# Optimization experiments

Measured on AMD Instinct MI355X. Metric: run time of the kernel, lower is better.

Reference implementation:

```python
import jax, jax.numpy as jnp
import numpy as np

T = 2048       # tokens (flattened, single causal sequence)
HID = 2048     # hidden_size
H = 16         # num_heads
DN = 128       # qk_nope_head_dim
DR = 64        # qk_rope_head_dim
DV = 128       # v_head_dim
DQK = DN + DR  # 192
QLR = 1536     # q_lora_rank
KVLR = 512     # kv_lora_rank
THETA = 10000.0
EPS = 1e-6
SCALE = DQK ** -0.5


def rmsnorm(x, w):
    return x * jax.lax.rsqrt(jnp.mean(x * x, axis=-1, keepdims=True) + EPS) * w


def rope_interleaved(x, cos, sin):
    # is_neox_style=False: rotate interleaved even/odd pairs
    x1 = x[..., 0::2]
    x2 = x[..., 1::2]
    out = jnp.stack([x1 * cos - x2 * sin, x2 * cos + x1 * sin], axis=-1)
    return out.reshape(x.shape)


def setup_inputs() -> dict:
    key = jax.random.key(0)
    ks = jax.random.split(key, 8)
    s = 0.02
    return {
        "positions": jnp.arange(T, dtype=jnp.int32),
        "hidden_states": jax.random.normal(ks[0], (T, HID), jnp.float32),
        "w_q_a": jax.random.normal(ks[1], (HID, QLR), jnp.float32) * s,
        "q_a_ln_w": jnp.ones((QLR,), jnp.float32),
        "w_q_b": jax.random.normal(ks[2], (QLR, H * DQK), jnp.float32) * s,
        "w_kv_a": jax.random.normal(ks[3], (HID, KVLR + DR), jnp.float32) * s,
        "kv_a_ln_w": jnp.ones((KVLR,), jnp.float32),
        "w_kv_b": jax.random.normal(ks[4], (KVLR, H * (DN + DV)), jnp.float32) * s,
        "w_o": jax.random.normal(ks[5], (H * DV, HID), jnp.float32) * s,
    }


def reference(positions, hidden_states, w_q_a, q_a_ln_w, w_q_b, w_kv_a,
              kv_a_ln_w, w_kv_b, w_o):
    t = hidden_states.shape[0]
    # --- Q low-rank path ---
    q = rmsnorm(hidden_states @ w_q_a, q_a_ln_w) @ w_q_b          # [T, H*DQK]
    q = q.reshape(t, H, DQK)
    q_nope, q_pe = q[..., :DN], q[..., DN:]
    # --- KV latent path ---
    latent = hidden_states @ w_kv_a                                # [T, KVLR+DR]
    kv_a = rmsnorm(latent[:, :KVLR], kv_a_ln_w)
    kv = (kv_a @ w_kv_b).reshape(t, H, DN + DV)
    k_nope, v = kv[..., :DN], kv[..., DN:]
    k_pe = latent[:, None, KVLR:]                                  # [T, 1, DR]
    # --- partial RoPE (non-neox, interleaved) ---
    inv_freq = 1.0 / (THETA ** (jnp.arange(0, DR, 2, dtype=jnp.float32) / DR))
    ang = positions.astype(jnp.float32)[:, None] * inv_freq        # [T, DR/2]
    cos = jnp.cos(ang)[:, None, :]
    sin = jnp.sin(ang)[:, None, :]
    q_pe = rope_interleaved(q_pe, cos, sin)
    k_pe = rope_interleaved(k_pe, cos, sin)
    q = jnp.concatenate([q_nope, q_pe], axis=-1)                   # [T, H, DQK]
    k = jnp.concatenate([k_nope, jnp.broadcast_to(k_pe, (t, H, DR))], axis=-1)
    # --- causal attention (V zero-padded to DQK then sliced == using V directly) ---
    scores = jnp.einsum("thd,shd->hts", q, k) * SCALE              # [H, T, T]
    causal = positions[None, :, None] >= positions[None, None, :]
    scores = jnp.where(causal, scores, jnp.finfo(scores.dtype).min)
    probs = jax.nn.softmax(scores, axis=-1)
    attn = jnp.einsum("hts,shd->thd", probs, v)                    # [T, H, DV]
    return attn.reshape(t, H * DV) @ w_o                           # [T, HID]
```

## Files before the change

kernel.cpp:

```cpp
#include <hip/hip_runtime.h>
#include <hip/hip_bf16.h>

#define T_ 2048
#define SCALE_ 0.07216878364870322f

typedef __bf16 bf16x8 __attribute__((ext_vector_type(8)));
typedef float f32x4 __attribute__((ext_vector_type(4)));
typedef float f32x16 __attribute__((ext_vector_type(16)));

__device__ inline bf16x8 load8f(const float* p) {
    const float4* f = reinterpret_cast<const float4*>(p);
    float4 a = f[0], b = f[1];
    bf16x8 r;
    r[0] = (__bf16)a.x; r[1] = (__bf16)a.y; r[2] = (__bf16)a.z; r[3] = (__bf16)a.w;
    r[4] = (__bf16)b.x; r[5] = (__bf16)b.y; r[6] = (__bf16)b.z; r[7] = (__bf16)b.w;
    return r;
}

__device__ inline void gld_lds16(const void* g, void* l) {
    __builtin_amdgcn_global_load_lds((const __attribute__((address_space(1))) void*)g,
                                     (__attribute__((address_space(3))) void*)l, 16, 0, 0);
}

__global__ __launch_bounds__(256) void cvt_bf16(const float* __restrict__ in,
                                                __bf16* __restrict__ out, int n8)
{
    int i = blockIdx.x * 256 + threadIdx.x;
    if (i < n8)
        *reinterpret_cast<bf16x8*>(out + (size_t)i * 8) = load8f(in + (size_t)i * 8);
}

__global__ __launch_bounds__(256) void transpose_cvt(
    const float* __restrict__ W, __bf16* __restrict__ Wt, int K, int N)
{
    __shared__ __bf16 tl[64][72];
    const int k0 = blockIdx.x * 64, n0 = blockIdx.y * 64;
    const int tid = threadIdx.x;
    const bool in = n0 < N;
    #pragma unroll
    for (int it = 0; it < 2; ++it) {
        int chunk = tid + it * 256;
        int r = chunk >> 3;
        int c8 = (chunk & 7) * 8;
        float4 a = {0,0,0,0}, b = {0,0,0,0};
        if (in) {
            const float* p = W + (size_t)(k0 + r) * N + n0 + c8;
            a = *reinterpret_cast<const float4*>(p);
            b = *reinterpret_cast<const float4*>(p + 4);
        }
        tl[c8+0][r] = (__bf16)a.x; tl[c8+1][r] = (__bf16)a.y;
        tl[c8+2][r] = (__bf16)a.z; tl[c8+3][r] = (__bf16)a.w;
        tl[c8+4][r] = (__bf16)b.x; tl[c8+5][r] = (__bf16)b.y;
        tl[c8+6][r] = (__bf16)b.z; tl[c8+7][r] = (__bf16)b.w;
    }
    __syncthreads();
    #pragma unroll
    for (int it = 0; it < 2; ++it) {
        int chunk = tid + it * 256;
        int n = chunk >> 3;
        int k8 = (chunk & 7) * 8;
        bf16x8 v = *reinterpret_cast<const bf16x8*>(&tl[n][k8]);
        *reinterpret_cast<bf16x8*>(Wt + (size_t)(n0 + n) * K + k0 + k8) = v;
    }
}

template <typename TC>
__global__ __launch_bounds__(256) void gemm_bt(
    const __bf16* __restrict__ A, const __bf16* __restrict__ Bt,
    TC* __restrict__ C, int M, int N, int K, int Nstore, int ldc)
{
    __shared__ __bf16 As[2][128 * 64];
    __shared__ __bf16 Bs[2][128 * 64];
    const int tid = threadIdx.x, lane = tid & 63, wid = tid >> 6;
    const int l15 = lane & 15, lg = lane >> 4;
    const int m0 = blockIdx.x * 128, n0 = blockIdx.y * 128;
    const int wr = (wid >> 1) * 64, wc = (wid & 1) * 64;

    const int srow = wid * 32 + (lane >> 3);
    const int scol = ((lane & 7) ^ (lane >> 3)) * 8;
    const __bf16* Ag = A  + (size_t)(m0 + srow) * K + scol;
    const __bf16* Bg = Bt + (size_t)(n0 + srow) * K + scol;
    const int lbase = wid * 4096;

    f32x4 acc[4][4] = {};

    {
        char* la = (char*)&As[0][0] + lbase;
        char* lb = (char*)&Bs[0][0] + lbase;
        #pragma unroll
        for (int i = 0; i < 4; ++i) {
            gld_lds16(Ag + (size_t)i * 8 * K, la + i * 1024);
            gld_lds16(Bg + (size_t)i * 8 * K, lb + i * 1024);
        }
    }
    __syncthreads();

    int cur = 0;
    for (int k0 = 0; k0 < K; k0 += 64) {
        if (k0 + 64 < K) {
            char* la = (char*)&As[cur ^ 1][0] + lbase;
            char* lb = (char*)&Bs[cur ^ 1][0] + lbase;
            #pragma unroll
            for (int i = 0; i < 4; ++i) {
                gld_lds16(Ag + (size_t)i * 8 * K + k0 + 64, la + i * 1024);
                gld_lds16(Bg + (size_t)i * 8 * K + k0 + 64, lb + i * 1024);
            }
        }

        bf16x8 af[4][2], bf[4][2];
        #pragma unroll
        for (int i = 0; i < 4; ++i) {
            const int Ra = wr + i * 16 + l15;
            const int Rb = wc + i * 16 + l15;
            const int ca = (lg ^ (Ra & 7)) * 16;
            const int cb = (lg ^ (Rb & 7)) * 16;
            const char* pa = (const char*)&As[cur][0] + Ra * 128;
            const char* pb = (const char*)&Bs[cur][0] + Rb * 128;
            af[i][0] = *reinterpret_cast<const bf16x8*>(pa + ca);
            af[i][1] = *reinterpret_cast<const bf16x8*>(pa + (ca ^ 64));
            bf[i][0] = *reinterpret_cast<const bf16x8*>(pb + cb);
            bf[i][1] = *reinterpret_cast<const bf16x8*>(pb + (cb ^ 64));
        }
        #pragma unroll
        for (int h = 0; h < 2; ++h)
            #pragma unroll
            for (int i = 0; i < 4; ++i)
                #pragma unroll
                for (int j = 0; j < 4; ++j)
                    acc[i][j] = __builtin_amdgcn_mfma_f32_16x16x32_bf16(af[i][h], bf[j][h], acc[i][j], 0, 0, 0);

        __syncthreads();
        cur ^= 1;
    }

    #pragma unroll
    for (int i = 0; i < 4; ++i)
        #pragma unroll
        for (int j = 0; j < 4; ++j)
            #pragma unroll
            for (int e = 0; e < 4; ++e) {
                int r = m0 + wr + i * 16 + lg * 4 + e;
                int c = n0 + wc + j * 16 + l15;
                if (c < Nstore)
                    C[(size_t)r * ldc + c] = (TC)acc[i][j][e];
            }
}

__global__ __launch_bounds__(256) void rmsnorm_k(
    const __bf16* __restrict__ in, int in_stride,
    const float* __restrict__ w,
    __bf16* __restrict__ out, int out_stride, int W)
{
    const int t = blockIdx.x, tid = threadIdx.x;
    const __bf16* row = in + (size_t)t * in_stride;
    float x[8];
    float ss = 0.f;
    const bool act = tid * 8 < W;
    if (act) {
        bf16x8 v = *reinterpret_cast<const bf16x8*>(row + tid * 8);
        #pragma unroll
        for (int e = 0; e < 8; ++e) { x[e] = (float)v[e]; ss += x[e] * x[e]; }
    }
    #pragma unroll
    for (int m = 1; m < 64; m <<= 1) ss += __shfl_xor(ss, m, 64);
    __shared__ float red[4];
    if ((tid & 63) == 0) red[tid >> 6] = ss;
    __syncthreads();
    float tot = red[0] + red[1] + red[2] + red[3];
    float scale = rsqrtf(tot / (float)W + 1e-6f);
    if (act) {
        float4 w0 = *reinterpret_cast<const float4*>(w + tid * 8);
        float4 w1 = *reinterpret_cast<const float4*>(w + tid * 8 + 4);
        bf16x8 o;
        o[0] = (__bf16)(x[0] * scale * w0.x); o[1] = (__bf16)(x[1] * scale * w0.y);
        o[2] = (__bf16)(x[2] * scale * w0.z); o[3] = (__bf16)(x[3] * scale * w0.w);
        o[4] = (__bf16)(x[4] * scale * w1.x); o[5] = (__bf16)(x[5] * scale * w1.y);
        o[6] = (__bf16)(x[6] * scale * w1.z); o[7] = (__bf16)(x[7] * scale * w1.w);
        *reinterpret_cast<bf16x8*>(out + (size_t)t * out_stride + tid * 8) = o;
    }
}

__global__ __launch_bounds__(256) void rope_q(
    const int* __restrict__ positions, __bf16* __restrict__ q)
{
    const int t = blockIdx.x, tid = threadIdx.x;
    __shared__ float cs[32], sn[32];
    if (tid < 32) {
        float pos = (float)positions[t];
        float invf = powf(10000.f, -(float)tid / 32.f);
        cs[tid] = cosf(pos * invf); sn[tid] = sinf(pos * invf);
    }
    __syncthreads();
    #pragma unroll
    for (int it = 0; it < 2; ++it) {
        int p = tid + it * 256;
        int h = p >> 5, i = p & 31;
        size_t base = (size_t)t * 3072 + h * 192 + 128 + 2 * i;
        float x1 = (float)q[base], x2 = (float)q[base + 1];
        q[base]     = (__bf16)(x1 * cs[i] - x2 * sn[i]);
        q[base + 1] = (__bf16)(x2 * cs[i] + x1 * sn[i]);
    }
}

__global__ __launch_bounds__(256) void kprep(
    const int* __restrict__ positions, const __bf16* __restrict__ kv,
    const __bf16* __restrict__ qkv_a, __bf16* __restrict__ kh)
{
    const int t = blockIdx.x, tid = threadIdx.x;
    __shared__ __bf16 kpe[64];
    if (tid < 32) {
        float pos = (float)positions[t];
        float invf = powf(10000.f, -(float)tid / 32.f);
        float c = cosf(pos * invf), s = sinf(pos * invf);
        float x1 = (float)qkv_a[(size_t)t * 2176 + 2048 + 2 * tid];
        float x2 = (float)qkv_a[(size_t)t * 2176 + 2049 + 2 * tid];
        kpe[2 * tid]     = (__bf16)(x1 * c - x2 * s);
        kpe[2 * tid + 1] = (__bf16)(x2 * c + x1 * s);
    }
    __syncthreads();
    const int h = tid >> 4, c = tid & 15;
    bf16x8 v = *reinterpret_cast<const bf16x8*>(kv + (size_t)t * 4096 + h * 256 + c * 8);
    *reinterpret_cast<bf16x8*>(kh + ((size_t)h * T_ + t) * 192 + c * 8) = v;
    if (c < 8) {
        bf16x8 p = *reinterpret_cast<const bf16x8*>(&kpe[c * 8]);
        *reinterpret_cast<bf16x8*>(kh + ((size_t)h * T_ + t) * 192 + 128 + c * 8) = p;
    }
}

__global__ __launch_bounds__(256) void vtrans(
    const __bf16* __restrict__ kv, __bf16* __restrict__ vt)
{
    __shared__ __bf16 tile[128][72];
    const int t0 = blockIdx.x * 64;
    const int h  = blockIdx.y;
    const int tid = threadIdx.x;
    #pragma unroll
    for (int it = 0; it < 4; ++it) {
        int chunk = tid + it * 256;
        int r = chunk >> 4;
        int d8 = (chunk & 15) * 8;
        bf16x8 v = *reinterpret_cast<const bf16x8*>(kv + (size_t)(t0 + r) * 4096 + h * 256 + 128 + d8);
        #pragma unroll
        for (int e = 0; e < 8; ++e) tile[d8 + e][r] = v[e];
    }
    __syncthreads();
    #pragma unroll
    for (int it = 0; it < 4; ++it) {
        int chunk = tid + it * 256;
        int d = chunk >> 3;
        int t8 = (chunk & 7) * 8;
        bf16x8 v = *reinterpret_cast<const bf16x8*>(&tile[d][t8]);
        *reinterpret_cast<bf16x8*>(vt + ((size_t)h * 128 + d) * 2048 + t0 + t8) = v;
    }
}

__device__ inline unsigned pk2(float a, float b) {
    union { __bf16 h[2]; unsigned u; } z;
    z.h[0] = (__bf16)a; z.h[1] = (__bf16)b;
    return z.u;
}

__global__ __launch_bounds__(512) void attn_flash(
    const __bf16* __restrict__ q, const __bf16* __restrict__ kh,
    const __bf16* __restrict__ vt, __bf16* __restrict__ attn)
{
    const int tid = threadIdx.x;
    const int lane = tid & 63, wid = tid >> 6;
    const int q31 = lane & 31, hi = lane >> 5;
    const int b = blockIdx.x;
    const int h = b & 15, x = b >> 4;
    const int g = wid >> 2;
    const int par = wid & 3;
    const int myqt = g ? (63 - x) : x;
    const int q0 = myqt * 32;

    __shared__ float mls[2][8][32];
    __shared__ float linv_s[2][32];
    __shared__ float obuf[2][32][129];

    const __bf16* Kh = kh + (size_t)h * T_ * 192;
    const __bf16* Vt = vt + (size_t)h * 128 * T_;
    const __bf16* Qp = q + (size_t)(q0 + q31) * 3072 + h * 192;

    bf16x8 aq[12];
    #pragma unroll
    for (int c = 0; c < 12; ++c)
        aq[c] = *reinterpret_cast<const bf16x8*>(Qp + c * 16 + hi * 8);

    f32x16 o[4] = {};
    float m_i = -1e30f, l_i = 0.f;
    const int ntile = myqt + 1;

    bf16x8 kc[12];
    if (par < ntile) {
        const __bf16* Kp = Kh + (size_t)(par * 32 + q31) * 192 + hi * 8;
        #pragma unroll
        for (int c = 0; c < 12; ++c)
            kc[c] = *reinterpret_cast<const bf16x8*>(Kp + c * 16);
    }

    for (int it = par; it < ntile; it += 4) {
        const int s0 = it * 32;

        bf16x8 vf[4][2];
        #pragma unroll
        for (int n = 0; n < 4; ++n)
            #pragma unroll
            for (int m = 0; m < 2; ++m)
                vf[n][m] = *reinterpret_cast<const bf16x8*>(
                    Vt + (size_t)(n * 32 + q31) * 2048 + s0 + (2 * m + hi) * 8);

        f32x16 sA = {}, sB = {};
        #pragma unroll
        for (int c = 0; c < 12; c += 2) {
            sA = __builtin_amdgcn_mfma_f32_32x32x16_bf16(kc[c],     aq[c],     sA, 0, 0, 0);
            sB = __builtin_amdgcn_mfma_f32_32x32x16_bf16(kc[c + 1], aq[c + 1], sB, 0, 0, 0);
        }

        bf16x8 kn[12];
        const bool notlast = (it + 4 < ntile);
        if (notlast) {
            const __bf16* Kp = Kh + (size_t)((it + 4) * 32 + q31) * 192 + hi * 8;
            #pragma unroll
            for (int c = 0; c < 12; ++c)
                kn[c] = *reinterpret_cast<const bf16x8*>(Kp + c * 16);
        }

        float v[16];
        #pragma unroll
        for (int r = 0; r < 16; ++r) v[r] = (sA[r] + sB[r]) * SCALE_;
        if (it == myqt) {
            #pragma unroll
            for (int r = 0; r < 16; ++r) {
                int crow = (r & 3) + 8 * (r >> 2) + 4 * hi;
                if (crow > q31) v[r] = -1e30f;
            }
        }
        float mx = v[0];
        #pragma unroll
        for (int r = 1; r < 16; ++r) mx = fmaxf(mx, v[r]);
        mx = fmaxf(mx, __shfl_xor(mx, 32, 64));
        const bool skip = __all(mx <= m_i);
        float mnew = fmaxf(m_i, mx);
        float fsc = skip ? 1.f : __expf(m_i - mnew);
        m_i = mnew;
        float ps = 0.f;
        #pragma unroll
        for (int r = 0; r < 16; ++r) { v[r] = __expf(v[r] - mnew); ps += v[r]; }
        ps += __shfl_xor(ps, 32, 64);
        l_i = l_i * fsc + ps;
        if (!skip) {
            #pragma unroll
            for (int n = 0; n < 4; ++n) o[n] *= fsc;
        }

        unsigned w[8], xw[8];
        #pragma unroll
        for (int i = 0; i < 8; ++i) w[i] = pk2(v[2 * i], v[2 * i + 1]);
        #pragma unroll
        for (int i = 0; i < 8; ++i) xw[i] = __shfl_xor(w[i], 32, 64);
        union { unsigned u[4]; bf16x8 v; } P0, P1;
        P0.u[0] = hi ? xw[2] : w[0]; P0.u[1] = hi ? xw[3] : w[1];
        P0.u[2] = hi ? w[2] : xw[0]; P0.u[3] = hi ? w[3] : xw[1];
        P1.u[0] = hi ? xw[6] : w[4]; P1.u[1] = hi ? xw[7] : w[5];
        P1.u[2] = hi ? w[6] : xw[4]; P1.u[3] = hi ? w[7] : xw[5];

        #pragma unroll
        for (int n = 0; n < 4; ++n) {
            o[n] = __builtin_amdgcn_mfma_f32_32x32x16_bf16(vf[n][0], P0.v, o[n], 0, 0, 0);
            o[n] = __builtin_amdgcn_mfma_f32_32x32x16_bf16(vf[n][1], P1.v, o[n], 0, 0, 0);
        }
        if (notlast) {
            #pragma unroll
            for (int c = 0; c < 12; ++c) kc[c] = kn[c];
        }
    }

    if (hi == 0) { mls[0][wid][q31] = m_i; mls[1][wid][q31] = l_i; }
    __syncthreads();
    const int gb = g * 4;
    float M = fmaxf(fmaxf(mls[0][gb][q31], mls[0][gb + 1][q31]),
                    fmaxf(mls[0][gb + 2][q31], mls[0][gb + 3][q31]));
    float L = mls[1][gb][q31]     * __expf(mls[0][gb][q31] - M)
            + mls[1][gb + 1][q31] * __expf(mls[0][gb + 1][q31] - M)
            + mls[1][gb + 2][q31] * __expf(mls[0][gb + 2][q31] - M)
            + mls[1][gb + 3][q31] * __expf(mls[0][gb + 3][q31] - M);
    float F = __expf(m_i - M);
    if (par == 0 && hi == 0) linv_s[g][q31] = 1.f / L;

    #pragma unroll
    for (int rd = 0; rd < 4; ++rd) {
        if (par == rd) {
            if (rd == 0) {
                #pragma unroll
                for (int n = 0; n < 4; ++n)
                    #pragma unroll
                    for (int r = 0; r < 16; ++r) {
                        int d = (r & 3) + 8 * (r >> 2) + 4 * hi + 32 * n;
                        obuf[g][q31][d] = F * o[n][r];
                    }
            } else {
                #pragma unroll
                for (int n = 0; n < 4; ++n)
                    #pragma unroll
                    for (int r = 0; r < 16; ++r) {
                        int d = (r & 3) + 8 * (r >> 2) + 4 * hi + 32 * n;
                        obuf[g][q31][d] += F * o[n][r];
                    }
            }
        }
        __syncthreads();
    }

    const int gtid = tid & 255;
    #pragma unroll
    for (int it = 0; it < 2; ++it) {
        int c = gtid + it * 256;
        int row = c >> 4, c8 = (c & 15) * 8;
        float inv = linv_s[g][row];
        bf16x8 vv;
        #pragma unroll
        for (int j = 0; j < 8; ++j)
            vv[j] = (__bf16)(obuf[g][row][c8 + j] * inv);
        *reinterpret_cast<bf16x8*>(attn + (size_t)(q0 + row) * 2048 + h * 128 + c8) = vv;
    }
}

extern "C" void kernel_launch(void* const* d_in, const int* in_sizes, int n_in,
                              void* d_out, int out_size, void* d_ws, size_t ws_size,
                              hipStream_t stream)
{
    const int*   positions = (const int*)d_in[0];
    const float* hidden    = (const float*)d_in[1];
    const float* w_q_a     = (const float*)d_in[2];
    const float* q_a_ln_w  = (const float*)d_in[3];
    const float* w_q_b     = (const float*)d_in[4];
    const float* w_kv_a    = (const float*)d_in[5];
    const float* kv_a_ln_w = (const float*)d_in[6];
    const float* w_kv_b    = (const float*)d_in[7];
    const float* w_o       = (const float*)d_in[8];

    char* ws = (char*)d_ws;
    __bf16* hidden_bf = (__bf16*)(ws);
    __bf16* vt        = (__bf16*)(ws);
    __bf16* wbuf      = (__bf16*)(ws + 8388608);
    __bf16* qkv_a     = (__bf16*)(ws + 17825792);
    __bf16* attn      = (__bf16*)(ws + 17825792);
    __bf16* q_a_n     = (__bf16*)(ws + 26738688);
    __bf16* q         = (__bf16*)(ws + 33030144);
    __bf16* kv_a_n    = (__bf16*)(ws + 45613056);
    __bf16* kv        = (__bf16*)(ws + 47710208);
    __bf16* kh        = (__bf16*)(ws + 64487424);

    dim3 blk(256);
    cvt_bf16<<<dim3(2048), blk, 0, stream>>>(hidden, hidden_bf, 524288);

    transpose_cvt<<<dim3(32, 24), blk, 0, stream>>>(w_q_a, wbuf, 2048, 1536);
    transpose_cvt<<<dim3(32, 10), blk, 0, stream>>>(w_kv_a, wbuf + (size_t)1536 * 2048, 2048, 576);
    gemm_bt<__bf16><<<dim3(16, 17), blk, 0, stream>>>(hidden_bf, wbuf, qkv_a, 2048, 2176, 2048, 2112, 2176);
    rmsnorm_k<<<dim3(2048), blk, 0, stream>>>(qkv_a, 2176, q_a_ln_w, q_a_n, 1536, 1536);
    rmsnorm_k<<<dim3(2048), blk, 0, stream>>>(qkv_a + 1536, 2176, kv_a_ln_w, kv_a_n, 512, 512);

    transpose_cvt<<<dim3(24, 48), blk, 0, stream>>>(w_q_b, wbuf, 1536, 3072);
    gemm_bt<__bf16><<<dim3(16, 24), blk, 0, stream>>>(q_a_n, wbuf, q, 2048, 3072, 1536, 3072, 3072);

    transpose_cvt<<<dim3(8, 64), blk, 0, stream>>>(w_kv_b, wbuf, 512, 4096);
    gemm_bt<__bf16><<<dim3(16, 32), blk, 0, stream>>>(kv_a_n, wbuf, kv, 2048, 4096, 512, 4096, 4096);

    rope_q<<<dim3(2048), blk, 0, stream>>>(positions, q);
    kprep<<<dim3(2048), blk, 0, stream>>>(positions, kv, qkv_a, kh);
    vtrans<<<dim3(32, 16), blk, 0, stream>>>(kv, vt);
    attn_flash<<<dim3(512), dim3(512), 0, stream>>>(q, kh, vt, attn);

    transpose_cvt<<<dim3(32, 32), blk, 0, stream>>>(w_o, wbuf, 2048, 2048);
    gemm_bt<float><<<dim3(16, 16), blk, 0, stream>>>(attn, wbuf, (float*)d_out, 2048, 2048, 2048, 2048, 2048);
}
```

Before: 259.0 us.

## Balance wave split between paired causal q-tiles and raise MFMA priority

Each block handles two query tiles (x and 63-x) with 8 waves. Before, the waves were split evenly 4/4, even though the short tile has far fewer KV tiles than the long one. Now the number of waves given to the first tile is proportional to its KV work, so both groups should finish at about the same time. The merge and reduction loops are generalized to variable group sizes, and the output writeback is redistributed across all threads. s_setprio is also raised around the MFMA blocks to favour matrix issue. A group can now reach 7 waves, which adds more merge sync rounds, and the first K load no longer checks whether its tile index is in range.

```diff
diff --git a/kernel.cpp b/kernel.cpp
--- a/kernel.cpp
+++ b/kernel.cpp
@@ -269,8 +269,10 @@
     const int q31 = lane & 31, hi = lane >> 5;
     const int b = blockIdx.x;
     const int h = b & 15, x = b >> 4;
-    const int g = wid >> 2;
-    const int par = wid & 3;
+    const int nA = max(1, min(7, (8 * (x + 1) + 32) / 65));
+    const int g = (wid < nA) ? 0 : 1;
+    const int par = g ? (wid - nA) : wid;
+    const int ngrp = g ? (8 - nA) : nA;
     const int myqt = g ? (63 - x) : x;
     const int q0 = myqt * 32;
 
@@ -292,14 +294,14 @@
     const int ntile = myqt + 1;
 
     bf16x8 kc[12];
-    if (par < ntile) {
+    {
         const __bf16* Kp = Kh + (size_t)(par * 32 + q31) * 192 + hi * 8;
         #pragma unroll
         for (int c = 0; c < 12; ++c)
             kc[c] = *reinterpret_cast<const bf16x8*>(Kp + c * 16);
     }
 
-    for (int it = par; it < ntile; it += 4) {
+    for (int it = par; it < ntile; it += ngrp) {
         const int s0 = it * 32;
 
         bf16x8 vf[4][2];
@@ -311,16 +313,18 @@
                     Vt + (size_t)(n * 32 + q31) * 2048 + s0 + (2 * m + hi) * 8);
 
         f32x16 sA = {}, sB = {};
+        __builtin_amdgcn_s_setprio(1);
         #pragma unroll
         for (int c = 0; c < 12; c += 2) {
             sA = __builtin_amdgcn_mfma_f32_32x32x16_bf16(kc[c],     aq[c],     sA, 0, 0, 0);
             sB = __builtin_amdgcn_mfma_f32_32x32x16_bf16(kc[c + 1], aq[c + 1], sB, 0, 0, 0);
         }
+        __builtin_amdgcn_s_setprio(0);
 
         bf16x8 kn[12];
-        const bool notlast = (it + 4 < ntile);
+        const bool notlast = (it + ngrp < ntile);
         if (notlast) {
-            const __bf16* Kp = Kh + (size_t)((it + 4) * 32 + q31) * 192 + hi * 8;
+            const __bf16* Kp = Kh + (size_t)((it + ngrp) * 32 + q31) * 192 + hi * 8;
             #pragma unroll
             for (int c = 0; c < 12; ++c)
                 kn[c] = *reinterpret_cast<const bf16x8*>(Kp + c * 16);
@@ -365,11 +369,13 @@
         P1.u[0] = hi ? xw[6] : w[4]; P1.u[1] = hi ? xw[7] : w[5];
         P1.u[2] = hi ? w[6] : xw[4]; P1.u[3] = hi ? w[7] : xw[5];
 
+        __builtin_amdgcn_s_setprio(1);
         #pragma unroll
         for (int n = 0; n < 4; ++n) {
             o[n] = __builtin_amdgcn_mfma_f32_32x32x16_bf16(vf[n][0], P0.v, o[n], 0, 0, 0);
             o[n] = __builtin_amdgcn_mfma_f32_32x32x16_bf16(vf[n][1], P1.v, o[n], 0, 0, 0);
         }
+        __builtin_amdgcn_s_setprio(0);
         if (notlast) {
             #pragma unroll
             for (int c = 0; c < 12; ++c) kc[c] = kn[c];
@@ -378,18 +384,16 @@
 
     if (hi == 0) { mls[0][wid][q31] = m_i; mls[1][wid][q31] = l_i; }
     __syncthreads();
-    const int gb = g * 4;
-    float M = fmaxf(fmaxf(mls[0][gb][q31], mls[0][gb + 1][q31]),
-                    fmaxf(mls[0][gb + 2][q31], mls[0][gb + 3][q31]));
-    float L = mls[1][gb][q31]     * __expf(mls[0][gb][q31] - M)
-            + mls[1][gb + 1][q31] * __expf(mls[0][gb + 1][q31] - M)
-            + mls[1][gb + 2][q31] * __expf(mls[0][gb + 2][q31] - M)
-            + mls[1][gb + 3][q31] * __expf(mls[0][gb + 3][q31] - M);
+    const int gb = g ? nA : 0;
+    float M = -1e30f;
+    for (int w = 0; w < ngrp; ++w) M = fmaxf(M, mls[0][gb + w][q31]);
+    float L = 0.f;
+    for (int w = 0; w < ngrp; ++w) L += mls[1][gb + w][q31] * __expf(mls[0][gb + w][q31] - M);
     float F = __expf(m_i - M);
     if (par == 0 && hi == 0) linv_s[g][q31] = 1.f / L;
 
     #pragma unroll
-    for (int rd = 0; rd < 4; ++rd) {
+    for (int rd = 0; rd < 7; ++rd) {
         if (par == rd) {
             if (rd == 0) {
                 #pragma unroll
@@ -412,17 +416,18 @@
         __syncthreads();
     }
 
-    const int gtid = tid & 255;
-    #pragma unroll
-    for (int it = 0; it < 2; ++it) {
-        int c = gtid + it * 256;
-        int row = c >> 4, c8 = (c & 15) * 8;
-        float inv = linv_s[g][row];
+    #pragma unroll
+    for (int it2 = 0; it2 < 2; ++it2) {
+        int c = tid + it2 * 512;
+        int gg = c >> 9;
+        int row = (c >> 4) & 31, c8 = (c & 15) * 8;
+        int qq0 = gg ? (63 - x) * 32 : x * 32;
+        float inv = linv_s[gg][row];
         bf16x8 vv;
         #pragma unroll
         for (int j = 0; j < 8; ++j)
-            vv[j] = (__bf16)(obuf[g][row][c8 + j] * inv);
-        *reinterpret_cast<bf16x8*>(attn + (size_t)(q0 + row) * 2048 + h * 128 + c8) = vv;
+            vv[j] = (__bf16)(obuf[gg][row][c8 + j] * inv);
+        *reinterpret_cast<bf16x8*>(attn + (size_t)(qq0 + row) * 2048 + h * 128 + c8) = vv;
     }
 }
 
```

Result: no change. 261.7 us (+1.0%).
